# Kernel tuning notes

Measured on AMD Instinct MI355X. Metric: run time of the kernel, lower is better.

## Reference

```python
import jax, jax.numpy as jnp
import numpy as np

N = 100000   # nodes
E = 300000   # directed edges
IN_DIM = 10
HID = 384
OUT_DIM = 3
T = 5
BN_EPS = 1e-5


def setup_inputs() -> dict:
    key = jax.random.key(0)
    ks = jax.random.split(key, 32)
    i = iter(range(32))
    nxt = lambda: ks[next(i)]
    d = {}
    d["x"] = jax.random.normal(nxt(), (N, IN_DIM), dtype=jnp.float32)
    d["edge_index"] = jax.random.randint(nxt(), (2, E), 0, N, dtype=jnp.int32)
    s = 0.05
    # SAGEConv layer 0 (in_dim -> hid); lin_l has bias, lin_r has no bias (PyG defaults)
    d["W_l0"] = jax.random.normal(nxt(), (HID, IN_DIM), dtype=jnp.float32) * s
    d["b_l0"] = jnp.zeros((HID,), dtype=jnp.float32)
    d["W_r0"] = jax.random.normal(nxt(), (HID, IN_DIM), dtype=jnp.float32) * s
    # SAGEConv layers 1..T-1 (hid -> hid), stacked
    d["W_l"] = jax.random.normal(nxt(), (T - 1, HID, HID), dtype=jnp.float32) * s
    d["b_l"] = jnp.zeros((T - 1, HID), dtype=jnp.float32)
    d["W_r"] = jax.random.normal(nxt(), (T - 1, HID, HID), dtype=jnp.float32) * s
    # per-layer BatchNorm (eval mode: running stats)
    d["bn_g"] = jnp.ones((T, HID), dtype=jnp.float32)
    d["bn_b"] = jnp.zeros((T, HID), dtype=jnp.float32)
    d["bn_m"] = jax.random.normal(nxt(), (T, HID), dtype=jnp.float32) * 0.1
    d["bn_v"] = jax.random.uniform(nxt(), (T, HID), dtype=jnp.float32, minval=0.5, maxval=1.5)
    # projection MLP: Linear->BN->ReLU->Linear->BN->ReLU->Linear
    d["Wp0"] = jax.random.normal(nxt(), (HID, HID), dtype=jnp.float32) * s
    d["bp0"] = jnp.zeros((HID,), dtype=jnp.float32)
    d["Wp1"] = jax.random.normal(nxt(), (HID, HID), dtype=jnp.float32) * s
    d["bp1"] = jnp.zeros((HID,), dtype=jnp.float32)
    d["Wp2"] = jax.random.normal(nxt(), (OUT_DIM, HID), dtype=jnp.float32) * s
    d["bp2"] = jnp.zeros((OUT_DIM,), dtype=jnp.float32)
    d["pbn_g"] = jnp.ones((2, HID), dtype=jnp.float32)
    d["pbn_b"] = jnp.zeros((2, HID), dtype=jnp.float32)
    d["pbn_m"] = jax.random.normal(nxt(), (2, HID), dtype=jnp.float32) * 0.1
    d["pbn_v"] = jax.random.uniform(nxt(), (2, HID), dtype=jnp.float32, minval=0.5, maxval=1.5)
    return d


def _bn(x, g, b, m, v):
    return (x - m) * jax.lax.rsqrt(v + BN_EPS) * g + b


def _sage(x, src, dst, Wl, bl, Wr):
    # mean aggregation of neighbor features, then lin_l(agg) + lin_r(x), L2-normalized
    msg = jax.ops.segment_sum(x[src], dst, num_segments=N)            # [N, F]
    cnt = jax.ops.segment_sum(jnp.ones_like(dst, dtype=x.dtype), dst, num_segments=N)
    agg = msg / jnp.maximum(cnt, 1.0)[:, None]
    out = agg @ Wl.T + bl + x @ Wr.T
    nrm = jnp.linalg.norm(out, axis=-1, keepdims=True)
    return out / jnp.maximum(nrm, 1e-12)


def reference(x, edge_index, W_l0, b_l0, W_r0, W_l, b_l, W_r,
              bn_g, bn_b, bn_m, bn_v,
              Wp0, bp0, Wp1, bp1, Wp2, bp2,
              pbn_g, pbn_b, pbn_m, pbn_v):
    src, dst = edge_index[0], edge_index[1]
    h = x
    for t in range(T):  # T=5, fixed small loop over structurally distinct layers
        if t == 0:
            h = _sage(h, src, dst, W_l0, b_l0, W_r0)
        else:
            h = _sage(h, src, dst, W_l[t - 1], b_l[t - 1], W_r[t - 1])
        h = jax.nn.elu(_bn(h, bn_g[t], bn_b[t], bn_m[t], bn_v[t]))
        # dropout is identity in eval mode
    # projection MLP
    h = jax.nn.relu(_bn(h @ Wp0.T + bp0, pbn_g[0], pbn_b[0], pbn_m[0], pbn_v[0]))
    h = jax.nn.relu(_bn(h @ Wp1.T + bp1, pbn_g[1], pbn_b[1], pbn_m[1], pbn_v[1]))
    return h @ Wp2.T + bp2  # [N, 3]
```

## Files before the change

kernel.cpp:

```cpp
#include <hip/hip_runtime.h>
#include <hip/hip_bf16.h>

#define N_NODES 100000
#define N_EDGES 300000
#define IN_DIM 10
#define HID 384
#define OUT_DIM 3
#define T_LAYERS 5
#define BN_EPS 1e-5f

typedef __attribute__((ext_vector_type(8))) short short8;
typedef __attribute__((ext_vector_type(4))) float floatx4;

__device__ __forceinline__ float bf16f(short v) {
  return __uint_as_float(((unsigned)(unsigned short)v) << 16);
}

__device__ __forceinline__ void gld_lds16(const void* g, void* l) {
  __builtin_amdgcn_global_load_lds(
      (const __attribute__((address_space(1))) void*)g,
      (__attribute__((address_space(3))) void*)l, 16, 0, 0);
}


__global__ void count_k(const int* __restrict__ dst, int* __restrict__ cnt, int E) {
  int e = blockIdx.x * blockDim.x + threadIdx.x;
  if (e < E) atomicAdd(&cnt[dst[e]], 1);
}

__global__ void scan_partial_k(const int* __restrict__ cnt, int* __restrict__ bsum, int n) {
  int t = threadIdx.x;
  int i = blockIdx.x * 1024 + t;
  int v = (i < n) ? cnt[i] : 0;
  #pragma unroll
  for (int off = 1; off < 64; off <<= 1) v += __shfl_xor(v, off);
  __shared__ int ws[16];
  if ((t & 63) == 0) ws[t >> 6] = v;
  __syncthreads();
  if (t == 0) {
    int s = 0;
    #pragma unroll
    for (int w = 0; w < 16; ++w) s += ws[w];
    bsum[blockIdx.x] = s;
  }
}

__global__ void scan_small_k(int* __restrict__ bsum, int P) {
  __shared__ int s[1024];
  int t = threadIdx.x;
  int v = (t < P) ? bsum[t] : 0;
  s[t] = v;
  __syncthreads();
  for (int off = 1; off < 1024; off <<= 1) {
    int add = (t >= off) ? s[t - off] : 0;
    __syncthreads();
    s[t] += add;
    __syncthreads();
  }
  if (t < P) bsum[t] = s[t] - v;
}

__global__ void scan_final_k(const int* __restrict__ cnt, const int* __restrict__ bsum,
                             int* __restrict__ row_off, int n) {
  int t = threadIdx.x, lane = t & 63, wv = t >> 6;
  int i = blockIdx.x * 1024 + t;
  int v = (i < n) ? cnt[i] : 0;
  int x = v;
  #pragma unroll
  for (int off = 1; off < 64; off <<= 1) {
    int y = __shfl_up(x, off);
    if (lane >= off) x += y;
  }
  __shared__ int ws[16];
  if (lane == 63) ws[wv] = x;
  __syncthreads();
  if (t == 0) {
    int a = 0;
    #pragma unroll
    for (int w = 0; w < 16; ++w) { int tmp = ws[w]; ws[w] = a; a += tmp; }
  }
  __syncthreads();
  int excl = (x - v) + ws[wv] + bsum[blockIdx.x];
  if (i <= n) row_off[i] = excl;
}

__global__ void fill_k(const int* __restrict__ src, const int* __restrict__ dst,
                       const int* __restrict__ row_off, int* __restrict__ cursor,
                       int* __restrict__ csr, int E) {
  int e = blockIdx.x * blockDim.x + threadIdx.x;
  if (e < E) {
    int d = dst[e];
    int pos = atomicAdd(&cursor[d], 1);
    csr[row_off[d] + pos] = src[e];
  }
}


__global__ void conv_k(const float* __restrict__ src, __hip_bfloat16* __restrict__ dst, int n) {
  int i = blockIdx.x * blockDim.x + threadIdx.x;
  if (i < n) dst[i] = __float2bfloat16(src[i]);
}

__global__ void pack0_k(const float* __restrict__ x, const float* __restrict__ agg10,
                        __hip_bfloat16* __restrict__ X2, int n) {
  int i = blockIdx.x * blockDim.x + threadIdx.x;
  if (i < n * 64) {
    int node = i >> 6, k = i & 63;
    float v = (k < IN_DIM) ? x[node * IN_DIM + k]
              : (k < 2 * IN_DIM) ? agg10[node * IN_DIM + (k - IN_DIM)] : 0.f;
    X2[i] = __float2bfloat16(v);
  }
}

__global__ void packw0_k(const float* __restrict__ Wl, const float* __restrict__ Wr,
                         __hip_bfloat16* __restrict__ W2) {
  int i = blockIdx.x * blockDim.x + threadIdx.x;
  if (i < HID * 64) {
    int o = i >> 6, k = i & 63;
    float v = (k < IN_DIM) ? Wr[o * IN_DIM + k]
              : (k < 2 * IN_DIM) ? Wl[o * IN_DIM + (k - IN_DIM)]
              : 0.f;
    W2[i] = __float2bfloat16(v);
  }
}


__global__ void agg10_k(const float* __restrict__ x, const int* __restrict__ row_off,
                        const int* __restrict__ csr, float* __restrict__ agg10, int n) {
  int sub = threadIdx.x >> 5;
  int lane = threadIdx.x & 31;
  int node = blockIdx.x * 8 + sub;
  if (node >= n) return;
  int s = row_off[node], e = row_off[node + 1];
  if (lane < IN_DIM) {
    float acc = 0.f;
    for (int j = s; j < e; ++j) acc += x[csr[j] * IN_DIM + lane];
    float c = (float)max(e - s, 1);
    agg10[node * IN_DIM + lane] = acc / c;
  }
}

__global__ __launch_bounds__(256) void aggv_k(const __hip_bfloat16* __restrict__ h,
                                              const int* __restrict__ row_off,
                                              const int* __restrict__ csr,
                                              __hip_bfloat16* __restrict__ agg, int n) {
  int node = blockIdx.x * 4 + (threadIdx.x >> 6);
  if (node >= n) return;
  int lane = threadIdx.x & 63;
  if (lane >= 48) return;
  int s = row_off[node], e = row_off[node + 1];
  float acc[8] = {0.f, 0.f, 0.f, 0.f, 0.f, 0.f, 0.f, 0.f};
  for (int j = s; j < e; ++j) {
    const uint4 v = *(const uint4*)(h + (size_t)csr[j] * HID + lane * 8);
    uint u0 = v.x, u1 = v.y, u2 = v.z, u3 = v.w;
    acc[0] += __uint_as_float(u0 << 16);
    acc[1] += __uint_as_float(u0 & 0xffff0000u);
    acc[2] += __uint_as_float(u1 << 16);
    acc[3] += __uint_as_float(u1 & 0xffff0000u);
    acc[4] += __uint_as_float(u2 << 16);
    acc[5] += __uint_as_float(u2 & 0xffff0000u);
    acc[6] += __uint_as_float(u3 << 16);
    acc[7] += __uint_as_float(u3 & 0xffff0000u);
  }
  float invc = 1.f / (float)max(e - s, 1);
  uint out[4];
  #pragma unroll
  for (int q = 0; q < 4; ++q) {
    __hip_bfloat16 lo = __float2bfloat16(acc[2 * q] * invc);
    __hip_bfloat16 hi = __float2bfloat16(acc[2 * q + 1] * invc);
    out[q] = (uint)(*(unsigned short*)&lo) | ((uint)(*(unsigned short*)&hi) << 16);
  }
  *(uint4*)(agg + (size_t)node * HID + lane * 8) = make_uint4(out[0], out[1], out[2], out[3]);
}

template <int KTOT, bool DUAL, int EPI, bool FINAL>
__global__ __launch_bounds__(512, 4) void mfma_gemm_k(
    const __hip_bfloat16* __restrict__ A1, const __hip_bfloat16* __restrict__ B1,
    const __hip_bfloat16* __restrict__ A2, const __hip_bfloat16* __restrict__ B2,
    const float* __restrict__ bias,
    const float* __restrict__ bng, const float* __restrict__ bnb,
    const float* __restrict__ bnm, const float* __restrict__ bnv,
    __hip_bfloat16* __restrict__ out,
    const float* __restrict__ W3, const float* __restrict__ b3,
    float* __restrict__ out3) {
  __shared__ alignas(16) short smem[32768];
  short* sB = smem + 8192;

  const int t = threadIdx.x;
  const int lane = t & 63;
  const int wv = t >> 6;
  const int n16 = lane & 15;
  const int quad = lane >> 4;
  const int row0 = blockIdx.x * 64;

  const int aRow = t >> 3;
  const int aG = (t & 7) ^ (aRow & 7);
  const int aOff = min(row0 + aRow, N_NODES - 1) * KTOT + aG * 8;
  int bOff[6];
  #pragma unroll
  for (int it = 0; it < 6; ++it) {
    int col = (wv * 6 + it) * 8 + (lane >> 3);
    int g = (lane & 7) ^ (col & 7);
    bOff[it] = col * KTOT + g * 8;
  }

  floatx4 acc[4][3];
  #pragma unroll
  for (int rt = 0; rt < 4; ++rt)
    #pragma unroll
    for (int ct = 0; ct < 3; ++ct) acc[rt][ct] = (floatx4)0.f;

  constexpr int KCH = KTOT / 64;
  constexpr int NCH = DUAL ? 2 * KCH : KCH;

  gld_lds16(A1 + aOff, smem + wv * 512);

  for (int c = 0; c < NCH; ++c) {
    const __hip_bfloat16* Bp;
    int kc;
    if (!DUAL || c < KCH) { Bp = B1; kc = c * 64; }
    else                  { Bp = B2; kc = (c - KCH) * 64; }

    #pragma unroll
    for (int it = 0; it < 6; ++it)
      gld_lds16(Bp + bOff[it] + kc, sB + (wv * 6 + it) * 512);

    if (c + 1 < NCH) {
      const __hip_bfloat16* Ap;
      int kn;
      int cn = c + 1;
      if (!DUAL || cn < KCH) { Ap = A1; kn = cn * 64; }
      else                   { Ap = A2; kn = (cn - KCH) * 64; }
      gld_lds16(Ap + aOff + kn, smem + (cn & 1) * 4096 + wv * 512);
      asm volatile("s_waitcnt vmcnt(1)" ::: "memory");
    } else {
      asm volatile("s_waitcnt vmcnt(0)" ::: "memory");
    }
    __builtin_amdgcn_sched_barrier(0);
    __builtin_amdgcn_s_barrier();

    const short* sAc = smem + (c & 1) * 4096;
    #pragma unroll
    for (int kh = 0; kh < 2; ++kh) {
      short8 af[4];
      int g = kh * 4 + quad;
      #pragma unroll
      for (int rt = 0; rt < 4; ++rt) {
        int r = rt * 16 + n16;
        af[rt] = *(const short8*)&sAc[r * 64 + ((g ^ (r & 7)) * 8)];
      }
      #pragma unroll
      for (int ct = 0; ct < 3; ++ct) {
        int cl = wv * 48 + ct * 16 + n16;
        short8 bf = *(const short8*)&sB[cl * 64 + ((g ^ (cl & 7)) * 8)];
        #pragma unroll
        for (int rt = 0; rt < 4; ++rt)
          acc[rt][ct] = __builtin_amdgcn_mfma_f32_16x16x32_bf16(af[rt], bf, acc[rt][ct], 0, 0, 0);
      }
    }
    __builtin_amdgcn_s_barrier();
    asm volatile("" ::: "memory");
  }

  int gc[3];
  #pragma unroll
  for (int ct = 0; ct < 3; ++ct) {
    gc[ct] = wv * 48 + ct * 16 + n16;
    float bs = bias[gc[ct]];
    #pragma unroll
    for (int rt = 0; rt < 4; ++rt)
      #pragma unroll
      for (int rg = 0; rg < 4; ++rg) acc[rt][ct][rg] += bs;
  }

  if constexpr (EPI == 0) {
    float* red = (float*)smem;
    #pragma unroll
    for (int rt = 0; rt < 4; ++rt)
      #pragma unroll
      for (int rg = 0; rg < 4; ++rg) {
        float s = 0.f;
        #pragma unroll
        for (int ct = 0; ct < 3; ++ct) s += acc[rt][ct][rg] * acc[rt][ct][rg];
        #pragma unroll
        for (int off = 1; off < 16; off <<= 1) s += __shfl_xor(s, off);
        if (n16 == 0) red[wv * 64 + rt * 16 + quad * 4 + rg] = s;
      }
    __syncthreads();
    #pragma unroll
    for (int rt = 0; rt < 4; ++rt) {
      float inv[4];
      #pragma unroll
      for (int rg = 0; rg < 4; ++rg) {
        int rl = rt * 16 + quad * 4 + rg;
        float ss = 0.f;
        #pragma unroll
        for (int w = 0; w < 8; ++w) ss += red[w * 64 + rl];
        inv[rg] = 1.f / fmaxf(sqrtf(ss), 1e-12f);
      }
      #pragma unroll
      for (int ct = 0; ct < 3; ++ct)
        #pragma unroll
        for (int rg = 0; rg < 4; ++rg) acc[rt][ct][rg] *= inv[rg];
    }
    __syncthreads();
  }

  constexpr int OS = 392;
  short* sO = smem;
  #pragma unroll
  for (int ct = 0; ct < 3; ++ct) {
    int col = gc[ct];
    float sc = bng[col] * rsqrtf(bnv[col] + BN_EPS);
    float sh = bnb[col] - bnm[col] * sc;
    #pragma unroll
    for (int rt = 0; rt < 4; ++rt)
      #pragma unroll
      for (int rg = 0; rg < 4; ++rg) {
        float xv = acc[rt][ct][rg] * sc + sh;
        if constexpr (EPI == 0)
          xv = xv > 0.f ? xv : expm1f(xv);
        else
          xv = fmaxf(xv, 0.f);
        __hip_bfloat16 bv = __float2bfloat16(xv);
        sO[(rt * 16 + quad * 4 + rg) * OS + col] = *(short*)&bv;
      }
  }
  __syncthreads();

  if constexpr (FINAL) {
    if (t < 192) {
      int row = t & 63, o = t >> 6;
      int grow = row0 + row;
      if (grow < N_NODES) {
        float s = 0.f;
        #pragma unroll
        for (int kb = 0; kb < 48; ++kb) {
          short8 hv = *(const short8*)&sO[row * OS + kb * 8];
          #pragma unroll
          for (int j = 0; j < 8; ++j) s += bf16f(hv[j]) * W3[o * HID + kb * 8 + j];
        }
        out3[grow * OUT_DIM + o] = s + b3[o];
      }
    }
  } else {
    #pragma unroll
    for (int it = 0; it < 6; ++it) {
      int e = t + it * 512;
      int row = e / 48, cs = e % 48;
      int grow = row0 + row;
      if (grow < N_NODES) {
        uint4 v = *(const uint4*)&sO[row * OS + cs * 8];
        *(uint4*)(out + (size_t)grow * HID + cs * 8) = v;
      }
    }
  }
}


extern "C" void kernel_launch(void* const* d_in, const int* in_sizes, int n_in,
                              void* d_out, int out_size, void* d_ws, size_t ws_size,
                              hipStream_t stream) {
  const float* x = (const float*)d_in[0];
  const int* ei = (const int*)d_in[1];
  const int* src = ei;
  const int* dst = ei + N_EDGES;
  const float* W_l0 = (const float*)d_in[2];
  const float* b_l0 = (const float*)d_in[3];
  const float* W_r0 = (const float*)d_in[4];
  const float* W_l = (const float*)d_in[5];
  const float* b_l = (const float*)d_in[6];
  const float* W_r = (const float*)d_in[7];
  const float* bn_g = (const float*)d_in[8];
  const float* bn_b = (const float*)d_in[9];
  const float* bn_m = (const float*)d_in[10];
  const float* bn_v = (const float*)d_in[11];
  const float* Wp0 = (const float*)d_in[12];
  const float* bp0 = (const float*)d_in[13];
  const float* Wp1 = (const float*)d_in[14];
  const float* bp1 = (const float*)d_in[15];
  const float* Wp2 = (const float*)d_in[16];
  const float* bp2 = (const float*)d_in[17];
  const float* pbn_g = (const float*)d_in[18];
  const float* pbn_b = (const float*)d_in[19];
  const float* pbn_m = (const float*)d_in[20];
  const float* pbn_v = (const float*)d_in[21];

  char* ws = (char*)d_ws;
  size_t off = 0;
  auto walloc = [&](size_t bytes) -> void* {
    void* p = ws + off;
    off = (off + bytes + 255) & ~(size_t)255;
    return p;
  };
  __hip_bfloat16* h   = (__hip_bfloat16*)walloc((size_t)N_NODES * HID * 2);
  __hip_bfloat16* agg = (__hip_bfloat16*)walloc((size_t)N_NODES * HID * 2);
  float* agg10 = (float*)agg;
  __hip_bfloat16* X2  = (__hip_bfloat16*)walloc((size_t)N_NODES * 64 * 2);
  __hip_bfloat16* W2  = (__hip_bfloat16*)walloc((size_t)HID * 64 * 2);
  __hip_bfloat16* WlB  = (__hip_bfloat16*)walloc((size_t)(T_LAYERS - 1) * HID * HID * 2);
  __hip_bfloat16* WrB  = (__hip_bfloat16*)walloc((size_t)(T_LAYERS - 1) * HID * HID * 2);
  __hip_bfloat16* Wp0B = (__hip_bfloat16*)walloc((size_t)HID * HID * 2);
  __hip_bfloat16* Wp1B = (__hip_bfloat16*)walloc((size_t)HID * HID * 2);
  int* cnt     = (int*)walloc((size_t)N_NODES * 4);
  int* row_off = (int*)walloc((size_t)(N_NODES + 1) * 4);
  int* cursor  = (int*)walloc((size_t)N_NODES * 4);
  int* csr     = (int*)walloc((size_t)N_EDGES * 4);
  int* bsum    = (int*)walloc(4096);

  hipMemsetAsync(cnt, 0, (size_t)N_NODES * 4, stream);
  hipMemsetAsync(cursor, 0, (size_t)N_NODES * 4, stream);

  const int NW = (T_LAYERS - 1) * HID * HID;
  conv_k<<<(NW + 255) / 256, 256, 0, stream>>>(W_l, WlB, NW);
  conv_k<<<(NW + 255) / 256, 256, 0, stream>>>(W_r, WrB, NW);
  conv_k<<<(HID * HID + 255) / 256, 256, 0, stream>>>(Wp0, Wp0B, HID * HID);
  conv_k<<<(HID * HID + 255) / 256, 256, 0, stream>>>(Wp1, Wp1B, HID * HID);
  packw0_k<<<(HID * 64 + 255) / 256, 256, 0, stream>>>(W_l0, W_r0, W2);

  count_k<<<(N_EDGES + 255) / 256, 256, 0, stream>>>(dst, cnt, N_EDGES);
  int P = (N_NODES + 1 + 1023) / 1024;
  scan_partial_k<<<P, 1024, 0, stream>>>(cnt, bsum, N_NODES);
  scan_small_k<<<1, 1024, 0, stream>>>(bsum, P);
  scan_final_k<<<P, 1024, 0, stream>>>(cnt, bsum, row_off, N_NODES);
  fill_k<<<(N_EDGES + 255) / 256, 256, 0, stream>>>(src, dst, row_off, cursor, csr, N_EDGES);

  const int GB = (N_NODES + 63) / 64;

  agg10_k<<<(N_NODES + 7) / 8, 256, 0, stream>>>(x, row_off, csr, agg10, N_NODES);
  pack0_k<<<(N_NODES * 64 + 255) / 256, 256, 0, stream>>>(x, agg10, X2, N_NODES);
  mfma_gemm_k<64, false, 0, false><<<GB, 512, 0, stream>>>(
      X2, W2, nullptr, nullptr, b_l0, bn_g, bn_b, bn_m, bn_v, h,
      nullptr, nullptr, nullptr);

  for (int t = 1; t < T_LAYERS; ++t) {
    aggv_k<<<(N_NODES + 3) / 4, 256, 0, stream>>>(h, row_off, csr, agg, N_NODES);
    mfma_gemm_k<HID, true, 0, false><<<GB, 512, 0, stream>>>(
        agg, WlB + (size_t)(t - 1) * HID * HID,
        h,   WrB + (size_t)(t - 1) * HID * HID,
        b_l + (size_t)(t - 1) * HID,
        bn_g + (size_t)t * HID, bn_b + (size_t)t * HID,
        bn_m + (size_t)t * HID, bn_v + (size_t)t * HID,
        h, nullptr, nullptr, nullptr);
  }

  mfma_gemm_k<HID, false, 1, false><<<GB, 512, 0, stream>>>(
      h, Wp0B, nullptr, nullptr, bp0, pbn_g, pbn_b, pbn_m, pbn_v, h,
      nullptr, nullptr, nullptr);
  mfma_gemm_k<HID, false, 1, true><<<GB, 512, 0, stream>>>(
      h, Wp1B, nullptr, nullptr, bp1, pbn_g + HID, pbn_b + HID, pbn_m + HID, pbn_v + HID, h,
      Wp2, bp2, (float*)d_out);
}
```

Measured before the change: 1.045 ms.

## Fuse neighbor aggregation into SAGE layer GEMM with ping-pong hidden buffers

Replaces the separate aggregation kernel plus dual GEMM for hidden layers with one kernel. Each 1024-thread block gathers and averages neighbor rows into shared memory, then runs the MFMA GEMM over both the self features and the aggregated tile, followed by the L2-normalize, BatchNorm and ELU epilogue. This removes the global write and re-read of the aggregated tensor and one launch per layer. Because neighbors are read from the previous layer while the output is written, two hidden buffers are alternated. The cost is about 112KB of shared memory per block, which limits occupancy, and the gather latency is no longer overlapped with other blocks' GEMM work in the same way.

```diff
diff --git a/kernel.cpp b/kernel.cpp
--- a/kernel.cpp
+++ b/kernel.cpp
@@ -138,39 +138,6 @@
     float c = (float)max(e - s, 1);
     agg10[node * IN_DIM + lane] = acc / c;
   }
-}
-
-__global__ __launch_bounds__(256) void aggv_k(const __hip_bfloat16* __restrict__ h,
-                                              const int* __restrict__ row_off,
-                                              const int* __restrict__ csr,
-                                              __hip_bfloat16* __restrict__ agg, int n) {
-  int node = blockIdx.x * 4 + (threadIdx.x >> 6);
-  if (node >= n) return;
-  int lane = threadIdx.x & 63;
-  if (lane >= 48) return;
-  int s = row_off[node], e = row_off[node + 1];
-  float acc[8] = {0.f, 0.f, 0.f, 0.f, 0.f, 0.f, 0.f, 0.f};
-  for (int j = s; j < e; ++j) {
-    const uint4 v = *(const uint4*)(h + (size_t)csr[j] * HID + lane * 8);
-    uint u0 = v.x, u1 = v.y, u2 = v.z, u3 = v.w;
-    acc[0] += __uint_as_float(u0 << 16);
-    acc[1] += __uint_as_float(u0 & 0xffff0000u);
-    acc[2] += __uint_as_float(u1 << 16);
-    acc[3] += __uint_as_float(u1 & 0xffff0000u);
-    acc[4] += __uint_as_float(u2 << 16);
-    acc[5] += __uint_as_float(u2 & 0xffff0000u);
-    acc[6] += __uint_as_float(u3 << 16);
-    acc[7] += __uint_as_float(u3 & 0xffff0000u);
-  }
-  float invc = 1.f / (float)max(e - s, 1);
-  uint out[4];
-  #pragma unroll
-  for (int q = 0; q < 4; ++q) {
-    __hip_bfloat16 lo = __float2bfloat16(acc[2 * q] * invc);
-    __hip_bfloat16 hi = __float2bfloat16(acc[2 * q + 1] * invc);
-    out[q] = (uint)(*(unsigned short*)&lo) | ((uint)(*(unsigned short*)&hi) << 16);
-  }
-  *(uint4*)(agg + (size_t)node * HID + lane * 8) = make_uint4(out[0], out[1], out[2], out[3]);
 }
 
 template <int KTOT, bool DUAL, int EPI, bool FINAL>
@@ -353,6 +320,198 @@
         uint4 v = *(const uint4*)&sO[row * OS + cs * 8];
         *(uint4*)(out + (size_t)grow * HID + cs * 8) = v;
       }
+    }
+  }
+}
+
+__global__ __launch_bounds__(1024, 4) void fused_sage_k(
+    const __hip_bfloat16* __restrict__ hsrc,
+    const int* __restrict__ row_off, const int* __restrict__ csr,
+    const __hip_bfloat16* __restrict__ Wl, const __hip_bfloat16* __restrict__ Wr,
+    const float* __restrict__ bias,
+    const float* __restrict__ bng, const float* __restrict__ bnb,
+    const float* __restrict__ bnm, const float* __restrict__ bnv,
+    __hip_bfloat16* __restrict__ hdst) {
+  __shared__ alignas(16) short smem[57344];
+  short* aggT = smem;
+  short* sB = smem + 24576;
+  short* sA = smem + 49152;
+
+  const int t = threadIdx.x;
+  const int lane = t & 63;
+  const int wv = t >> 6;
+  const int n16 = lane & 15;
+  const int quad = lane >> 4;
+  const int row0 = blockIdx.x * 64;
+
+  int aOff = 0;
+  if (wv < 8) {
+    int r = wv * 8 + (lane >> 3);
+    int g = (lane & 7) ^ (r & 7);
+    aOff = min(row0 + r, N_NODES - 1) * HID + g * 8;
+    gld_lds16(hsrc + aOff, sA + wv * 512);
+  }
+
+  int bOff[3];
+  #pragma unroll
+  for (int it = 0; it < 3; ++it) {
+    int col = (wv * 3 + it) * 8 + (lane >> 3);
+    int g = (lane & 7) ^ (col & 7);
+    bOff[it] = col * HID + g * 8;
+  }
+
+  if (lane < 48) {
+    #pragma unroll 1
+    for (int i = 0; i < 4; ++i) {
+      int r = wv * 4 + i;
+      int node = row0 + r;
+      int dcol = (lane >> 3) * 64 + (((lane & 7) ^ (r & 7)) * 8);
+      uint o0 = 0, o1 = 0, o2 = 0, o3 = 0;
+      if (node < N_NODES) {
+        int s = row_off[node], e = row_off[node + 1];
+        float a0 = 0, a1 = 0, a2 = 0, a3 = 0, a4 = 0, a5 = 0, a6 = 0, a7 = 0;
+        for (int j = s; j < e; ++j) {
+          const uint4 v = *(const uint4*)(hsrc + (size_t)csr[j] * HID + lane * 8);
+          a0 += __uint_as_float(v.x << 16); a1 += __uint_as_float(v.x & 0xffff0000u);
+          a2 += __uint_as_float(v.y << 16); a3 += __uint_as_float(v.y & 0xffff0000u);
+          a4 += __uint_as_float(v.z << 16); a5 += __uint_as_float(v.z & 0xffff0000u);
+          a6 += __uint_as_float(v.w << 16); a7 += __uint_as_float(v.w & 0xffff0000u);
+        }
+        float invc = 1.f / (float)max(e - s, 1);
+        __hip_bfloat16 b0 = __float2bfloat16(a0 * invc), b1 = __float2bfloat16(a1 * invc);
+        __hip_bfloat16 b2 = __float2bfloat16(a2 * invc), b3 = __float2bfloat16(a3 * invc);
+        __hip_bfloat16 b4 = __float2bfloat16(a4 * invc), b5 = __float2bfloat16(a5 * invc);
+        __hip_bfloat16 b6 = __float2bfloat16(a6 * invc), b7 = __float2bfloat16(a7 * invc);
+        o0 = (uint)(*(unsigned short*)&b0) | ((uint)(*(unsigned short*)&b1) << 16);
+        o1 = (uint)(*(unsigned short*)&b2) | ((uint)(*(unsigned short*)&b3) << 16);
+        o2 = (uint)(*(unsigned short*)&b4) | ((uint)(*(unsigned short*)&b5) << 16);
+        o3 = (uint)(*(unsigned short*)&b6) | ((uint)(*(unsigned short*)&b7) << 16);
+      }
+      *(uint4*)&aggT[r * HID + dcol] = make_uint4(o0, o1, o2, o3);
+    }
+  }
+  __syncthreads();
+
+  const int wr = wv >> 3, wc = wv & 7;
+  floatx4 acc[2][3];
+  #pragma unroll
+  for (int rt = 0; rt < 2; ++rt)
+    #pragma unroll
+    for (int ct = 0; ct < 3; ++ct) acc[rt][ct] = (floatx4)0.f;
+
+  #pragma unroll
+  for (int c = 0; c < 12; ++c) {
+    const __hip_bfloat16* Bp = (c < 6) ? Wr : Wl;
+    const int kc = (c < 6 ? c : c - 6) * 64;
+
+    #pragma unroll
+    for (int it = 0; it < 3; ++it)
+      gld_lds16(Bp + bOff[it] + kc, sB + (wv * 3 + it) * 512);
+
+    const bool pf = (wv < 8) && (c + 1 < 6);
+    if (pf) {
+      gld_lds16(hsrc + aOff + (c + 1) * 64, sA + ((c + 1) & 1) * 4096 + wv * 512);
+      asm volatile("s_waitcnt vmcnt(1)" ::: "memory");
+    } else {
+      asm volatile("s_waitcnt vmcnt(0)" ::: "memory");
+    }
+    __builtin_amdgcn_sched_barrier(0);
+    __builtin_amdgcn_s_barrier();
+
+    #pragma unroll
+    for (int kh = 0; kh < 2; ++kh) {
+      short8 af[2];
+      int g = kh * 4 + quad;
+      #pragma unroll
+      for (int rt = 0; rt < 2; ++rt) {
+        int r = wr * 32 + rt * 16 + n16;
+        if (c < 6)
+          af[rt] = *(const short8*)&sA[(c & 1) * 4096 + r * 64 + ((g ^ (r & 7)) * 8)];
+        else
+          af[rt] = *(const short8*)&aggT[r * HID + kc + ((g ^ (r & 7)) * 8)];
+      }
+      #pragma unroll
+      for (int ct = 0; ct < 3; ++ct) {
+        int cl = wc * 48 + ct * 16 + n16;
+        short8 bf = *(const short8*)&sB[cl * 64 + ((g ^ (cl & 7)) * 8)];
+        #pragma unroll
+        for (int rt = 0; rt < 2; ++rt)
+          acc[rt][ct] = __builtin_amdgcn_mfma_f32_16x16x32_bf16(af[rt], bf, acc[rt][ct], 0, 0, 0);
+      }
+    }
+    __builtin_amdgcn_s_barrier();
+    asm volatile("" ::: "memory");
+  }
+
+  int gc[3];
+  #pragma unroll
+  for (int ct = 0; ct < 3; ++ct) {
+    gc[ct] = wc * 48 + ct * 16 + n16;
+    float bs = bias[gc[ct]];
+    #pragma unroll
+    for (int rt = 0; rt < 2; ++rt)
+      #pragma unroll
+      for (int rg = 0; rg < 4; ++rg) acc[rt][ct][rg] += bs;
+  }
+
+  float* red = (float*)sA;
+  #pragma unroll
+  for (int rt = 0; rt < 2; ++rt)
+    #pragma unroll
+    for (int rg = 0; rg < 4; ++rg) {
+      float s = 0.f;
+      #pragma unroll
+      for (int ct = 0; ct < 3; ++ct) s += acc[rt][ct][rg] * acc[rt][ct][rg];
+      #pragma unroll
+      for (int off = 1; off < 16; off <<= 1) s += __shfl_xor(s, off);
+      if (n16 == 0) red[wv * 32 + rt * 16 + quad * 4 + rg] = s;
+    }
+  __syncthreads();
+  #pragma unroll
+  for (int rt = 0; rt < 2; ++rt) {
+    float inv[4];
+    #pragma unroll
+    for (int rg = 0; rg < 4; ++rg) {
+      int lr = rt * 16 + quad * 4 + rg;
+      float ss = 0.f;
+      #pragma unroll
+      for (int w8 = 0; w8 < 8; ++w8) ss += red[(wr * 8 + w8) * 32 + lr];
+      inv[rg] = 1.f / fmaxf(sqrtf(ss), 1e-12f);
+    }
+    #pragma unroll
+    for (int ct = 0; ct < 3; ++ct)
+      #pragma unroll
+      for (int rg = 0; rg < 4; ++rg) acc[rt][ct][rg] *= inv[rg];
+  }
+  __syncthreads();
+
+  constexpr int OS = 392;
+  short* sO = smem;
+  #pragma unroll
+  for (int ct = 0; ct < 3; ++ct) {
+    int col = gc[ct];
+    float sc = bng[col] * rsqrtf(bnv[col] + BN_EPS);
+    float sh = bnb[col] - bnm[col] * sc;
+    #pragma unroll
+    for (int rt = 0; rt < 2; ++rt)
+      #pragma unroll
+      for (int rg = 0; rg < 4; ++rg) {
+        float xv = acc[rt][ct][rg] * sc + sh;
+        xv = xv > 0.f ? xv : expm1f(xv);
+        __hip_bfloat16 bv = __float2bfloat16(xv);
+        sO[(wr * 32 + rt * 16 + quad * 4 + rg) * OS + col] = *(short*)&bv;
+      }
+  }
+  __syncthreads();
+
+  #pragma unroll
+  for (int it = 0; it < 3; ++it) {
+    int e = t + it * 1024;
+    int row = e / 48, cs = e % 48;
+    int grow = row0 + row;
+    if (grow < N_NODES) {
+      uint4 v = *(const uint4*)&sO[row * OS + cs * 8];
+      *(uint4*)(hdst + (size_t)grow * HID + cs * 8) = v;
     }
   }
 }
@@ -393,9 +552,9 @@
     off = (off + bytes + 255) & ~(size_t)255;
     return p;
   };
-  __hip_bfloat16* h   = (__hip_bfloat16*)walloc((size_t)N_NODES * HID * 2);
-  __hip_bfloat16* agg = (__hip_bfloat16*)walloc((size_t)N_NODES * HID * 2);
-  float* agg10 = (float*)agg;
+  __hip_bfloat16* h0  = (__hip_bfloat16*)walloc((size_t)N_NODES * HID * 2);
+  __hip_bfloat16* h1  = (__hip_bfloat16*)walloc((size_t)N_NODES * HID * 2);
+  float* agg10 = (float*)h1;
   __hip_bfloat16* X2  = (__hip_bfloat16*)walloc((size_t)N_NODES * 64 * 2);
   __hip_bfloat16* W2  = (__hip_bfloat16*)walloc((size_t)HID * 64 * 2);
   __hip_bfloat16* WlB  = (__hip_bfloat16*)walloc((size_t)(T_LAYERS - 1) * HID * HID * 2);
@@ -430,24 +589,27 @@
   agg10_k<<<(N_NODES + 7) / 8, 256, 0, stream>>>(x, row_off, csr, agg10, N_NODES);
   pack0_k<<<(N_NODES * 64 + 255) / 256, 256, 0, stream>>>(x, agg10, X2, N_NODES);
   mfma_gemm_k<64, false, 0, false><<<GB, 512, 0, stream>>>(
-      X2, W2, nullptr, nullptr, b_l0, bn_g, bn_b, bn_m, bn_v, h,
+      X2, W2, nullptr, nullptr, b_l0, bn_g, bn_b, bn_m, bn_v, h0,
       nullptr, nullptr, nullptr);
 
+  __hip_bfloat16* hin = h0;
+  __hip_bfloat16* hout = h1;
   for (int t = 1; t < T_LAYERS; ++t) {
-    aggv_k<<<(N_NODES + 3) / 4, 256, 0, stream>>>(h, row_off, csr, agg, N_NODES);
-    mfma_gemm_k<HID, true, 0, false><<<GB, 512, 0, stream>>>(
-        agg, WlB + (size_t)(t - 1) * HID * HID,
-        h,   WrB + (size_t)(t - 1) * HID * HID,
+    fused_sage_k<<<GB, 1024, 0, stream>>>(
+        hin, row_off, csr,
+        WlB + (size_t)(t - 1) * HID * HID,
+        WrB + (size_t)(t - 1) * HID * HID,
         b_l + (size_t)(t - 1) * HID,
         bn_g + (size_t)t * HID, bn_b + (size_t)t * HID,
         bn_m + (size_t)t * HID, bn_v + (size_t)t * HID,
-        h, nullptr, nullptr, nullptr);
+        hout);
+    __hip_bfloat16* tmp = hin; hin = hout; hout = tmp;
   }
 
   mfma_gemm_k<HID, false, 1, false><<<GB, 512, 0, stream>>>(
-      h, Wp0B, nullptr, nullptr, bp0, pbn_g, pbn_b, pbn_m, pbn_v, h,
+      hin, Wp0B, nullptr, nullptr, bp0, pbn_g, pbn_b, pbn_m, pbn_v, hin,
       nullptr, nullptr, nullptr);
   mfma_gemm_k<HID, false, 1, true><<<GB, 512, 0, stream>>>(
-      h, Wp1B, nullptr, nullptr, bp1, pbn_g + HID, pbn_b + HID, pbn_m + HID, pbn_v + HID, h,
+      hin, Wp1B, nullptr, nullptr, bp1, pbn_g + HID, pbn_b + HID, pbn_m + HID, pbn_v + HID, hin,
       Wp2, bp2, (float*)d_out);
 }
```

Result: slower. 1.309 ms (+25.2%).

## Enlarge GEMM tile to 128 rows with 16 waves and double-buffered weights

Applied to the files above, without the earlier changes.

The fused SAGE/MLP GEMM now processes 128 rows per block with 1024 threads, arranged as a 2x8 wave grid, instead of 64 rows with 512 threads. Each weight chunk loaded into LDS is therefore reused across twice as many rows, which halves weight traffic per output row. The weight tile is also double-buffered alongside the activation tile, so the next chunk's loads overlap with the current chunk's MFMAs instead of running serially behind a barrier. In exchange, LDS use per block grows to 128KB, which likely allows only one block per CU. Larger blocks also mean coarser scheduling and a heavier tail.

```diff
diff --git a/kernel.cpp b/kernel.cpp
--- a/kernel.cpp
+++ b/kernel.cpp
@@ -174,7 +174,7 @@
 }
 
 template <int KTOT, bool DUAL, int EPI, bool FINAL>
-__global__ __launch_bounds__(512, 4) void mfma_gemm_k(
+__global__ __launch_bounds__(1024, 4) void mfma_gemm_k(
     const __hip_bfloat16* __restrict__ A1, const __hip_bfloat16* __restrict__ B1,
     const __hip_bfloat16* __restrict__ A2, const __hip_bfloat16* __restrict__ B2,
     const float* __restrict__ bias,
@@ -183,27 +183,28 @@
     __hip_bfloat16* __restrict__ out,
     const float* __restrict__ W3, const float* __restrict__ b3,
     float* __restrict__ out3) {
-  __shared__ alignas(16) short smem[32768];
-  short* sB = smem + 8192;
+  __shared__ alignas(16) short smem[65536];
 
   const int t = threadIdx.x;
   const int lane = t & 63;
   const int wv = t >> 6;
   const int n16 = lane & 15;
   const int quad = lane >> 4;
-  const int row0 = blockIdx.x * 64;
+  const int row0 = blockIdx.x * 128;
 
   const int aRow = t >> 3;
   const int aG = (t & 7) ^ (aRow & 7);
   const int aOff = min(row0 + aRow, N_NODES - 1) * KTOT + aG * 8;
-  int bOff[6];
-  #pragma unroll
-  for (int it = 0; it < 6; ++it) {
-    int col = (wv * 6 + it) * 8 + (lane >> 3);
+  int bOff[3];
+  #pragma unroll
+  for (int it = 0; it < 3; ++it) {
+    int col = (wv * 3 + it) * 8 + (lane >> 3);
     int g = (lane & 7) ^ (col & 7);
     bOff[it] = col * KTOT + g * 8;
   }
 
+  const int wr = wv >> 3, wc = wv & 7;
+
   floatx4 acc[4][3];
   #pragma unroll
   for (int rt = 0; rt < 4; ++rt)
@@ -213,46 +214,47 @@
   constexpr int KCH = KTOT / 64;
   constexpr int NCH = DUAL ? 2 * KCH : KCH;
 
-  gld_lds16(A1 + aOff, smem + wv * 512);
-
-  for (int c = 0; c < NCH; ++c) {
+  auto stage = [&](int c) {
+    const __hip_bfloat16* Ap;
     const __hip_bfloat16* Bp;
     int kc;
-    if (!DUAL || c < KCH) { Bp = B1; kc = c * 64; }
-    else                  { Bp = B2; kc = (c - KCH) * 64; }
-
-    #pragma unroll
-    for (int it = 0; it < 6; ++it)
-      gld_lds16(Bp + bOff[it] + kc, sB + (wv * 6 + it) * 512);
-
+    if (!DUAL || c < KCH) { Ap = A1; Bp = B1; kc = c * 64; }
+    else                  { Ap = A2; Bp = B2; kc = (c - KCH) * 64; }
+    short* sAb = smem + (c & 1) * 8192;
+    short* sBb = smem + 16384 + (c & 1) * 24576;
+    #pragma unroll
+    for (int it = 0; it < 3; ++it)
+      gld_lds16(Bp + bOff[it] + kc, sBb + (wv * 3 + it) * 512);
+    gld_lds16(Ap + aOff + kc, sAb + wv * 512);
+  };
+
+  stage(0);
+
+  for (int c = 0; c < NCH; ++c) {
     if (c + 1 < NCH) {
-      const __hip_bfloat16* Ap;
-      int kn;
-      int cn = c + 1;
-      if (!DUAL || cn < KCH) { Ap = A1; kn = cn * 64; }
-      else                   { Ap = A2; kn = (cn - KCH) * 64; }
-      gld_lds16(Ap + aOff + kn, smem + (cn & 1) * 4096 + wv * 512);
-      asm volatile("s_waitcnt vmcnt(1)" ::: "memory");
+      stage(c + 1);
+      asm volatile("s_waitcnt vmcnt(4)" ::: "memory");
     } else {
       asm volatile("s_waitcnt vmcnt(0)" ::: "memory");
     }
     __builtin_amdgcn_sched_barrier(0);
     __builtin_amdgcn_s_barrier();
 
-    const short* sAc = smem + (c & 1) * 4096;
+    const short* sAc = smem + (c & 1) * 8192;
+    const short* sBc = smem + 16384 + (c & 1) * 24576;
     #pragma unroll
     for (int kh = 0; kh < 2; ++kh) {
       short8 af[4];
       int g = kh * 4 + quad;
       #pragma unroll
       for (int rt = 0; rt < 4; ++rt) {
-        int r = rt * 16 + n16;
+        int r = wr * 64 + rt * 16 + n16;
         af[rt] = *(const short8*)&sAc[r * 64 + ((g ^ (r & 7)) * 8)];
       }
       #pragma unroll
       for (int ct = 0; ct < 3; ++ct) {
-        int cl = wv * 48 + ct * 16 + n16;
-        short8 bf = *(const short8*)&sB[cl * 64 + ((g ^ (cl & 7)) * 8)];
+        int cl = wc * 48 + ct * 16 + n16;
+        short8 bf = *(const short8*)&sBc[cl * 64 + ((g ^ (cl & 7)) * 8)];
         #pragma unroll
         for (int rt = 0; rt < 4; ++rt)
           acc[rt][ct] = __builtin_amdgcn_mfma_f32_16x16x32_bf16(af[rt], bf, acc[rt][ct], 0, 0, 0);
@@ -265,7 +267,7 @@
   int gc[3];
   #pragma unroll
   for (int ct = 0; ct < 3; ++ct) {
-    gc[ct] = wv * 48 + ct * 16 + n16;
+    gc[ct] = wc * 48 + ct * 16 + n16;
     float bs = bias[gc[ct]];
     #pragma unroll
     for (int rt = 0; rt < 4; ++rt)
@@ -292,10 +294,10 @@
       float inv[4];
       #pragma unroll
       for (int rg = 0; rg < 4; ++rg) {
-        int rl = rt * 16 + quad * 4 + rg;
+        int lr = rt * 16 + quad * 4 + rg;
         float ss = 0.f;
         #pragma unroll
-        for (int w = 0; w < 8; ++w) ss += red[w * 64 + rl];
+        for (int w8 = 0; w8 < 8; ++w8) ss += red[(wr * 8 + w8) * 64 + lr];
         inv[rg] = 1.f / fmaxf(sqrtf(ss), 1e-12f);
       }
       #pragma unroll
@@ -323,14 +325,14 @@
         else
           xv = fmaxf(xv, 0.f);
         __hip_bfloat16 bv = __float2bfloat16(xv);
-        sO[(rt * 16 + quad * 4 + rg) * OS + col] = *(short*)&bv;
+        sO[(wr * 64 + rt * 16 + quad * 4 + rg) * OS + col] = *(short*)&bv;
       }
   }
   __syncthreads();
 
   if constexpr (FINAL) {
-    if (t < 192) {
-      int row = t & 63, o = t >> 6;
+    if (t < 384) {
+      int row = t & 127, o = t >> 7;
       int grow = row0 + row;
       if (grow < N_NODES) {
         float s = 0.f;
@@ -346,7 +348,7 @@
   } else {
     #pragma unroll
     for (int it = 0; it < 6; ++it) {
-      int e = t + it * 512;
+      int e = t + it * 1024;
       int row = e / 48, cs = e % 48;
       int grow = row0 + row;
       if (grow < N_NODES) {
@@ -425,17 +427,17 @@
   scan_final_k<<<P, 1024, 0, stream>>>(cnt, bsum, row_off, N_NODES);
   fill_k<<<(N_EDGES + 255) / 256, 256, 0, stream>>>(src, dst, row_off, cursor, csr, N_EDGES);
 
-  const int GB = (N_NODES + 63) / 64;
+  const int GB = (N_NODES + 127) / 128;
 
   agg10_k<<<(N_NODES + 7) / 8, 256, 0, stream>>>(x, row_off, csr, agg10, N_NODES);
   pack0_k<<<(N_NODES * 64 + 255) / 256, 256, 0, stream>>>(x, agg10, X2, N_NODES);
-  mfma_gemm_k<64, false, 0, false><<<GB, 512, 0, stream>>>(
+  mfma_gemm_k<64, false, 0, false><<<GB, 1024, 0, stream>>>(
       X2, W2, nullptr, nullptr, b_l0, bn_g, bn_b, bn_m, bn_v, h,
       nullptr, nullptr, nullptr);
 
   for (int t = 1; t < T_LAYERS; ++t) {
     aggv_k<<<(N_NODES + 3) / 4, 256, 0, stream>>>(h, row_off, csr, agg, N_NODES);
-    mfma_gemm_k<HID, true, 0, false><<<GB, 512, 0, stream>>>(
+    mfma_gemm_k<HID, true, 0, false><<<GB, 1024, 0, stream>>>(
         agg, WlB + (size_t)(t - 1) * HID * HID,
         h,   WrB + (size_t)(t - 1) * HID * HID,
         b_l + (size_t)(t - 1) * HID,
@@ -444,10 +446,10 @@
         h, nullptr, nullptr, nullptr);
   }
 
-  mfma_gemm_k<HID, false, 1, false><<<GB, 512, 0, stream>>>(
+  mfma_gemm_k<HID, false, 1, false><<<GB, 1024, 0, stream>>>(
       h, Wp0B, nullptr, nullptr, bp0, pbn_g, pbn_b, pbn_m, pbn_v, h,
       nullptr, nullptr, nullptr);
-  mfma_gemm_k<HID, false, 1, true><<<GB, 512, 0, stream>>>(
+  mfma_gemm_k<HID, false, 1, true><<<GB, 1024, 0, stream>>>(
       h, Wp1B, nullptr, nullptr, bp1, pbn_g + HID, pbn_b + HID, pbn_m + HID, pbn_v + HID, h,
       Wp2, bp2, (float*)d_out);
 }
```

New measurement: 1.130 ms. 1.08x slower.
